# Kernel tuning notes

Measured on AMD Instinct MI355X. Metric: run time of the kernel, lower is better.

The kernel has to match this reference:

```python
import jax, jax.numpy as jnp
import numpy as np

B, N, DIM, VDIM, H, HD = 4, 1369, 1024, 1536, 16, 64
ROPE_HW, ROPE_DIM, THETA = 37, 32, 10000.0
LN_EPS = 1e-5


def _rope_tables():
    # VisionRotaryEmbeddingFast: freqs_for='lang', dim=32, pt_seq_len=ft_seq_len=37
    inv = 1.0 / THETA ** (jnp.arange(0, ROPE_DIM, 2, dtype=jnp.float32) / ROPE_DIM)  # [16]
    t = jnp.arange(ROPE_HW, dtype=jnp.float32) / ROPE_HW * ROPE_HW                    # [37]
    f = t[:, None] * inv[None, :]                                                     # [37,16]
    f = jnp.repeat(f, 2, axis=-1)                                                     # [37,32]
    # broadcat along last dim over the 2D grid -> [37,37,64]
    f2 = jnp.concatenate([jnp.broadcast_to(f[:, None, :], (ROPE_HW, ROPE_HW, ROPE_DIM)),
                          jnp.broadcast_to(f[None, :, :], (ROPE_HW, ROPE_HW, ROPE_DIM))], axis=-1)
    f2 = f2.reshape(-1, 2 * ROPE_DIM)                                                 # [1369,64]
    return jnp.cos(f2), jnp.sin(f2)


def _rotate_half(x):
    # pairs (x0,x1) -> (-x1,x0), interleaved
    xr = x.reshape(*x.shape[:-1], x.shape[-1] // 2, 2)
    x1, x2 = xr[..., 0], xr[..., 1]
    return jnp.stack((-x2, x1), axis=-1).reshape(x.shape)


def setup_inputs() -> dict:
    key = jax.random.key(0)
    ks = jax.random.split(key, 8)
    return {
        "x": jax.random.normal(ks[0], (B, N, DIM), jnp.float32),
        "value": jax.random.normal(ks[1], (B, N, VDIM), jnp.float32),
        "attn_mask": jax.random.randint(ks[2], (B, N), 0, 2).astype(bool),
        "wq": jax.random.normal(ks[3], (DIM, DIM), jnp.float32) * 0.02,
        "wk": jax.random.normal(ks[4], (DIM, VDIM), jnp.float32) * 0.02,
        "wv": jax.random.normal(ks[5], (DIM, VDIM), jnp.float32) * 0.02,
        "ln_g": jnp.ones((DIM,), jnp.float32),
        "ln_b": jnp.zeros((DIM,), jnp.float32),
        "wp": jax.random.normal(ks[6], (DIM, DIM), jnp.float32) * 0.02,
        "bp": jnp.zeros((DIM,), jnp.float32),
    }


def reference(x, value, attn_mask, wq, wk, wv, ln_g, ln_b, wp, bp):
    cos, sin = _rope_tables()  # [N, 64] each
    # projections (torch F.linear: y = x @ W.T)
    q = jnp.einsum('bni,oi->bno', x, wq).reshape(B, N, H, HD).transpose(0, 2, 1, 3)
    k = jnp.einsum('bni,oi->bno', value, wk).reshape(B, N, H, HD).transpose(0, 2, 1, 3)
    v = jnp.einsum('bni,oi->bno', value, wv).reshape(B, N, H, HD).transpose(0, 2, 1, 3)
    # inline RoPE on q and k
    q = q * cos + _rotate_half(q) * sin
    k = k * cos + _rotate_half(k) * sin
    q = q * (HD ** -0.5)
    attn = jnp.einsum('bhnd,bhmd->bhnm', q, k)
    neg_inf = jnp.finfo(attn.dtype).min
    attn = jnp.where(attn_mask[:, None, None, :], attn, neg_inf)
    attn = jax.nn.softmax(attn, axis=-1)
    out = jnp.einsum('bhnm,bhmd->bhnd', attn, v)
    out = out.transpose(0, 2, 1, 3).reshape(B, N, H * HD)
    # inner_attn_ln (LayerNorm, eps=1e-5)
    mu = jnp.mean(out, axis=-1, keepdims=True)
    var = jnp.var(out, axis=-1, keepdims=True)
    out = (out - mu) * jax.lax.rsqrt(var + LN_EPS) * ln_g + ln_b
    # output projection
    return jnp.einsum('bni,oi->bno', out, wp) + bp
```

## Files before the change

kernel.cpp:

```cpp
#include <hip/hip_runtime.h>
#include <hip/hip_bf16.h>

#define BB 4
#define NN 1369
#define DIMM 1024
#define VDIMM 1536
#define HH 16
#define MM (BB*NN)
#define MPAD 5504
#define NPAD 1408
#define KVB 64
#define NT (NPAD/KVB)

typedef __attribute__((ext_vector_type(4))) float f32x4;
typedef __attribute__((ext_vector_type(8))) __bf16 bf16x8;
typedef __attribute__((ext_vector_type(4))) __bf16 bf16x4;

#define GLOAD_LDS(gsrc, ldst) \
  __builtin_amdgcn_global_load_lds((const __attribute__((address_space(1))) unsigned int*)(gsrc), \
                                   (__attribute__((address_space(3))) unsigned int*)(ldst), 16, 0, 0)

__global__ __launch_bounds__(256) void cvt4(const float* __restrict__ src,
                                            __bf16* __restrict__ dst, int n4) {
  int i = blockIdx.x * blockDim.x + threadIdx.x;
  int st = gridDim.x * blockDim.x;
  for (; i < n4; i += st) {
    f32x4 v = ((const f32x4*)src)[i];
    bf16x4 o;
    o[0] = (__bf16)v[0]; o[1] = (__bf16)v[1];
    o[2] = (__bf16)v[2]; o[3] = (__bf16)v[3];
    ((bf16x4*)dst)[i] = o;
  }
}

__global__ __launch_bounds__(256) void rope_tables(float* __restrict__ cosT,
                                                   float* __restrict__ sinT) {
  int idx = blockIdx.x * blockDim.x + threadIdx.x;
  if (idx >= NN * 64) return;
  int n = idx >> 6, d = idx & 63;
  int r = n / 37, c = n % 37;
  int m = (d < 32) ? (d >> 1) : ((d - 32) >> 1);
  float p = (d < 32) ? (float)r : (float)c;
  float inv = powf(10000.f, -(float)m * (1.f / 16.f));
  float a = p * inv;
  cosT[idx] = cosf(a);
  sinT[idx] = sinf(a);
}

__global__ __launch_bounds__(256) void mask_prep(const void* __restrict__ mask,
                                                 float* __restrict__ maskA) {
  __shared__ int flags[2];
  int t = threadIdx.x;
  if (t < 2) flags[t] = 0;
  __syncthreads();
  const unsigned int* mw = (const unsigned int*)mask;
  for (int i = t; i < NN; i += blockDim.x) {
    unsigned int w = mw[i];
    if (w == 0x3F800000u) atomicOr(&flags[1], 1);
    else if (w > 1u) atomicOr(&flags[0], 1);
  }
  __syncthreads();
  int md = flags[1] ? 2 : (flags[0] ? 1 : 0);
  const unsigned char* mb = (const unsigned char*)mask;
  const float* mf = (const float*)mask;
  for (int i = t; i < BB * NPAD; i += blockDim.x) {
    int b = i / NPAD, key = i % NPAD;
    float v = -1e30f;
    if (key < NN) {
      int idx = b * NN + key;
      bool on = (md == 0) ? (mw[idx] != 0u) : (md == 1) ? (mb[idx] != 0) : (mf[idx] != 0.f);
      if (on) v = 0.f;
    }
    maskA[i] = v;
  }
}

template <int EPI>
__global__ __launch_bounds__(256) void gemm_bt(
    const __bf16* __restrict__ A, const __bf16* __restrict__ W, int K,
    __bf16* __restrict__ obf, float* __restrict__ of32,
    const float* __restrict__ cosT, const float* __restrict__ sinT,
    const float* __restrict__ bp) {
  __shared__ __bf16 As[128 * 32];
  __shared__ __bf16 Bs[128 * 32];
  const int tid = threadIdx.x;
  const int w = tid >> 6, l = tid & 63;
  const int tM = blockIdx.y, tN = blockIdx.x;
  const int wm = w >> 1, wn = w & 1;
  const int lo = l & 15, hi = l >> 4;

  f32x4 zero = {0.f, 0.f, 0.f, 0.f};
  f32x4 acc[4][4];
#pragma unroll
  for (int i = 0; i < 4; ++i)
#pragma unroll
    for (int j = 0; j < 4; ++j) acc[i][j] = zero;

  for (int k0 = 0; k0 < K; k0 += 32) {
    __syncthreads();
#pragma unroll
    for (int j = 0; j < 2; ++j) {
      int c = j * 4 + w;
      {
        const char* src = (const char*)A +
            ((size_t)(tM * 128 + c * 16 + (l >> 2)) * K + k0) * 2 + (l & 3) * 16;
        GLOAD_LDS(src, (char*)As + c * 1024);
      }
      {
        const char* src = (const char*)W +
            ((size_t)(tN * 128 + c * 16 + (l >> 2)) * K + k0) * 2 + (l & 3) * 16;
        GLOAD_LDS(src, (char*)Bs + c * 1024);
      }
    }
    __syncthreads();
    bf16x8 af[4], bfr[4];
#pragma unroll
    for (int mi = 0; mi < 4; ++mi)
      af[mi] = *(const bf16x8*)&As[(wm * 64 + mi * 16 + lo) * 32 + hi * 8];
#pragma unroll
    for (int ni = 0; ni < 4; ++ni)
      bfr[ni] = *(const bf16x8*)&Bs[(wn * 64 + ni * 16 + lo) * 32 + hi * 8];
#pragma unroll
    for (int mi = 0; mi < 4; ++mi)
#pragma unroll
      for (int ni = 0; ni < 4; ++ni)
        acc[mi][ni] = __builtin_amdgcn_mfma_f32_16x16x32_bf16(af[mi], bfr[ni], acc[mi][ni], 0, 0, 0);
  }

  const int m_base = tM * 128 + wm * 64;
  const int o_base = tN * 128 + wn * 64;
#pragma unroll
  for (int mi = 0; mi < 4; ++mi) {
#pragma unroll
    for (int r = 0; r < 4; ++r) {
      const int mrow = m_base + mi * 16 + hi * 4 + r;
#pragma unroll
      for (int ni = 0; ni < 4; ++ni) {
        const int col = o_base + ni * 16 + lo;
        float v = acc[mi][ni][r];
        if (EPI == 0 || EPI == 1) {
          float pprt = __shfl_xor(v, 1);
          if (mrow < MM) {
            int b = mrow / NN, n = mrow % NN;
            int h = col >> 6, d = col & 63;
            float cs = cosT[n * 64 + d], sn = sinT[n * 64 + d];
            float out = v * cs + (((d & 1) == 0) ? -pprt : pprt) * sn;
            if (EPI == 0) out *= 0.125f;
            obf[((size_t)(b * HH + h) * NPAD + n) * 64 + d] = (__bf16)out;
          }
        } else if (EPI == 2) {
          if (mrow < MM) {
            int b = mrow / NN, n = mrow % NN;
            int h = col >> 6, d = col & 63;
            obf[((size_t)(b * HH + h) * 64 + d) * NPAD + n] = (__bf16)v;
          }
        } else {
          if (mrow < MM) of32[(size_t)mrow * DIMM + col] = v + bp[col];
        }
      }
    }
  }
}

__device__ inline unsigned int pk2(float a, float b) {
  unsigned int ua = (unsigned int)__builtin_bit_cast(unsigned short, (__bf16)a);
  unsigned int ub = (unsigned int)__builtin_bit_cast(unsigned short, (__bf16)b);
  return ua | (ub << 16);
}

__global__ __launch_bounds__(256) void attn_kernel(
    const __bf16* __restrict__ Qb, const __bf16* __restrict__ Kb,
    const __bf16* __restrict__ Vtb, const float* __restrict__ maskA,
    float* __restrict__ AO) {
  __shared__ __bf16 Ks[2][64 * 64];
  __shared__ __bf16 Vs[2][64 * 64];
  __shared__ unsigned int Plds[4][16 * 32];
  const int tid = threadIdx.x;
  const int w = tid >> 6, l = tid & 63;
  const int lo = l & 15, hi = l >> 4;

  const int i = blockIdx.x;
  const int orig = (i & 7) * 176 + (i >> 3);
  const int bh = orig / NT;
  const int qt = orig % NT;
  const int b = bh >> 4;
  const int q0 = qt * 64 + w * 16;

  const __bf16* Qp = Qb + ((size_t)bh * NPAD + q0) * 64;
  bf16x8 qf0 = *(const bf16x8*)&Qp[lo * 64 + hi * 8];
  bf16x8 qf1 = *(const bf16x8*)&Qp[lo * 64 + 32 + hi * 8];

  const int row8 = l >> 3;
  const int swz16 = ((l & 7) ^ row8) << 4;
  const int lo7 = lo & 7;
  const int swzW = (lo & 7) << 2;

  f32x4 zero = {0.f, 0.f, 0.f, 0.f};
  f32x4 O[4];
#pragma unroll
  for (int n = 0; n < 4; ++n) O[n] = zero;
  float lr = 0.f;
  const float* mk = maskA + b * NPAD;

#define STAGE(buf, k0)                                                                   \
  {                                                                                      \
    _Pragma("unroll") for (int j = 0; j < 2; ++j) {                                      \
      const int rbase = (j * 4 + w) * 8;                                                 \
      const char* ksrc = (const char*)Kb +                                               \
          ((size_t)bh * NPAD + (k0) + rbase + row8) * 128 + swz16;                       \
      GLOAD_LDS(ksrc, (char*)&Ks[buf][0] + rbase * 128);                                 \
      const char* vsrc = (const char*)Vtb +                                              \
          ((size_t)(bh * 64 + rbase + row8) * NPAD + (k0)) * 2 + swz16;                  \
      GLOAD_LDS(vsrc, (char*)&Vs[buf][0] + rbase * 128);                                 \
    }                                                                                    \
  }

  STAGE(0, 0);
  __syncthreads();
  int cur = 0;

  for (int t = 0; t < NT; ++t) {
    if (t + 1 < NT) STAGE(cur ^ 1, (t + 1) * KVB);

    const __bf16* KB = &Ks[cur][0];
    const __bf16* VB = &Vs[cur][0];

    f32x4 mv[4];
#pragma unroll
    for (int c = 0; c < 4; ++c) mv[c] = *(const f32x4*)&mk[t * KVB + c * 16 + hi * 4];

    f32x4 S[4];
    __builtin_amdgcn_s_setprio(1);
#pragma unroll
    for (int c = 0; c < 4; ++c) {
      const int kr = c * 16 + lo;
      bf16x8 kfa = *(const bf16x8*)&KB[kr * 64 + ((hi ^ lo7) * 8)];
      bf16x8 kfb = *(const bf16x8*)&KB[kr * 64 + (((hi + 4) ^ lo7) * 8)];
      f32x4 s = __builtin_amdgcn_mfma_f32_16x16x32_bf16(kfa, qf0, zero, 0, 0, 0);
      S[c]     = __builtin_amdgcn_mfma_f32_16x16x32_bf16(kfb, qf1, s, 0, 0, 0);
    }
    __builtin_amdgcn_s_setprio(0);

    float rs = 0.f;
#pragma unroll
    for (int c = 0; c < 4; ++c) {
      float p0 = __expf(S[c][0] + mv[c][0]);
      float p1 = __expf(S[c][1] + mv[c][1]);
      float p2 = __expf(S[c][2] + mv[c][2]);
      float p3 = __expf(S[c][3] + mv[c][3]);
      rs += (p0 + p1) + (p2 + p3);
      uint2 pw = {pk2(p0, p1), pk2(p2, p3)};
      *(uint2*)&Plds[w][lo * 32 + ((8 * c + 2 * hi) ^ swzW)] = pw;
    }
    lr += rs;

    bf16x8 pf0 = *(const bf16x8*)&Plds[w][lo * 32 + ((4 * hi) ^ swzW)];
    bf16x8 pf1 = *(const bf16x8*)&Plds[w][lo * 32 + ((16 + 4 * hi) ^ swzW)];

    __builtin_amdgcn_s_setprio(1);
#pragma unroll
    for (int n = 0; n < 4; ++n) {
      const int vr = n * 16 + lo;
      bf16x8 vfa = *(const bf16x8*)&VB[vr * 64 + ((hi ^ lo7) * 8)];
      bf16x8 vfb = *(const bf16x8*)&VB[vr * 64 + (((hi + 4) ^ lo7) * 8)];
      O[n] = __builtin_amdgcn_mfma_f32_16x16x32_bf16(vfa, pf0, O[n], 0, 0, 0);
      O[n] = __builtin_amdgcn_mfma_f32_16x16x32_bf16(vfb, pf1, O[n], 0, 0, 0);
    }
    __builtin_amdgcn_s_setprio(0);

    __syncthreads();
    cur ^= 1;
  }
#undef STAGE

  lr += __shfl_xor(lr, 16);
  lr += __shfl_xor(lr, 32);
  const float inv = 1.f / lr;

  const int h = bh & 15;
  const int token = q0 + lo;
  if (token < NN) {
    float* dst = AO + (size_t)(b * NN + token) * DIMM + h * 64 + hi * 4;
#pragma unroll
    for (int n = 0; n < 4; ++n) {
      f32x4 o = O[n];
      o[0] *= inv; o[1] *= inv; o[2] *= inv; o[3] *= inv;
      *(f32x4*)(dst + n * 16) = o;
    }
  }
}

__global__ __launch_bounds__(256) void ln_kernel(
    const float* __restrict__ AO, const float* __restrict__ g,
    const float* __restrict__ be, __bf16* __restrict__ outb) {
  const int row = blockIdx.x;
  const int t = threadIdx.x;
  const float* x = AO + (size_t)row * DIMM;
  f32x4 v = ((const f32x4*)x)[t];
  float s = v[0] + v[1] + v[2] + v[3];
  float sq = v[0] * v[0] + v[1] * v[1] + v[2] * v[2] + v[3] * v[3];
#pragma unroll
  for (int m = 1; m < 64; m <<= 1) { s += __shfl_xor(s, m); sq += __shfl_xor(sq, m); }
  __shared__ float ss[4], ssq[4];
  int w = t >> 6, l = t & 63;
  if (l == 0) { ss[w] = s; ssq[w] = sq; }
  __syncthreads();
  s = ss[0] + ss[1] + ss[2] + ss[3];
  sq = ssq[0] + ssq[1] + ssq[2] + ssq[3];
  float mean = s * (1.f / 1024.f);
  float var = sq * (1.f / 1024.f) - mean * mean;
  float rstd = rsqrtf(var + 1e-5f);
  __bf16* o = outb + (size_t)row * DIMM + t * 4;
  const float* gp = g + t * 4;
  const float* bp2 = be + t * 4;
#pragma unroll
  for (int j = 0; j < 4; ++j) o[j] = (__bf16)((v[j] - mean) * rstd * gp[j] + bp2[j]);
}

extern "C" void kernel_launch(void* const* d_in, const int* in_sizes, int n_in,
                              void* d_out, int out_size, void* d_ws, size_t ws_size,
                              hipStream_t stream) {
  const float* x   = (const float*)d_in[0];
  const float* val = (const float*)d_in[1];
  const void*  msk = d_in[2];
  const float* wq  = (const float*)d_in[3];
  const float* wk  = (const float*)d_in[4];
  const float* wv  = (const float*)d_in[5];
  const float* lng = (const float*)d_in[6];
  const float* lnb = (const float*)d_in[7];
  const float* wp  = (const float*)d_in[8];
  const float* bpv = (const float*)d_in[9];
  float* out = (float*)d_out;

  char* ws = (char*)d_ws;
  size_t off = 0;
  auto alloc = [&](size_t bytes) -> char* {
    char* p = ws + off;
    off += (bytes + 255) & ~(size_t)255;
    return p;
  };
  __bf16* xb  = (__bf16*)alloc((size_t)MPAD * 1024 * 2);
  __bf16* vb  = (__bf16*)alloc((size_t)MPAD * 1536 * 2);
  __bf16* wqb = (__bf16*)alloc((size_t)1024 * 1024 * 2);
  __bf16* wkb = (__bf16*)alloc((size_t)1024 * 1536 * 2);
  __bf16* wvb = (__bf16*)alloc((size_t)1024 * 1536 * 2);
  __bf16* wpb = (__bf16*)alloc((size_t)1024 * 1024 * 2);
  __bf16* Qb  = (__bf16*)alloc((size_t)64 * NPAD * 64 * 2);
  __bf16* Kb  = (__bf16*)alloc((size_t)64 * NPAD * 64 * 2);
  __bf16* Vtb = (__bf16*)alloc((size_t)64 * 64 * NPAD * 2);
  float* AO   = (float*)alloc((size_t)MM * 1024 * 4);
  float* cosT = (float*)alloc((size_t)NN * 64 * 4);
  float* sinT = (float*)alloc((size_t)NN * 64 * 4);
  float* maskA = (float*)alloc((size_t)BB * NPAD * 4);

  hipMemsetAsync(xb + (size_t)MM * 1024, 0, (size_t)(MPAD - MM) * 1024 * 2, stream);
  hipMemsetAsync(vb + (size_t)MM * 1536, 0, (size_t)(MPAD - MM) * 1536 * 2, stream);
  hipMemsetAsync(Qb, 0, (size_t)64 * NPAD * 64 * 2, stream);
  hipMemsetAsync(Kb, 0, (size_t)64 * NPAD * 64 * 2, stream);
  hipMemsetAsync(Vtb, 0, (size_t)64 * 64 * NPAD * 2, stream);

  cvt4<<<1024, 256, 0, stream>>>(x, xb, MM * 1024 / 4);
  cvt4<<<1024, 256, 0, stream>>>(val, vb, MM * 1536 / 4);
  cvt4<<<512, 256, 0, stream>>>(wq, wqb, 1024 * 1024 / 4);
  cvt4<<<512, 256, 0, stream>>>(wk, wkb, 1024 * 1536 / 4);
  cvt4<<<512, 256, 0, stream>>>(wv, wvb, 1024 * 1536 / 4);
  cvt4<<<512, 256, 0, stream>>>(wp, wpb, 1024 * 1024 / 4);
  rope_tables<<<(NN * 64 + 255) / 256, 256, 0, stream>>>(cosT, sinT);
  mask_prep<<<1, 256, 0, stream>>>(msk, maskA);

  dim3 gg(8, 43);
  gemm_bt<0><<<gg, 256, 0, stream>>>(xb, wqb, 1024, Qb, nullptr, cosT, sinT, nullptr);
  gemm_bt<1><<<gg, 256, 0, stream>>>(vb, wkb, 1536, Kb, nullptr, cosT, sinT, nullptr);
  gemm_bt<2><<<gg, 256, 0, stream>>>(vb, wvb, 1536, Vtb, nullptr, nullptr, nullptr, nullptr);

  attn_kernel<<<dim3(64 * NT), 256, 0, stream>>>(Qb, Kb, Vtb, maskA, AO);

  ln_kernel<<<MM, 256, 0, stream>>>(AO, lng, lnb, xb);

  gemm_bt<3><<<gg, 256, 0, stream>>>(xb, wpb, 1024, nullptr, out, nullptr, nullptr, bpv);
}
```

Baseline: 314.1 us.

## Fuse K and V projections into one GEMM, use 64-wide tiles, exp2 softmax

The separate K and V projection GEMMs become one GEMM over a concatenated [2048,1536] weight. Its epilogue sends columns below 1024 to the RoPE'd K output and the rest to the transposed V output. The Q and output-projection GEMMs switch to 128x64 tiles, giving a 16x43 grid that fills more CUs. The Q scale now folds in log2(e), so the attention softmax can use exp2f instead of __expf. Smaller tiles mean each block reuses less data per load.

```diff
diff --git a/kernel.cpp b/kernel.cpp
--- a/kernel.cpp
+++ b/kernel.cpp
@@ -11,6 +11,7 @@
 #define NPAD 1408
 #define KVB 64
 #define NT (NPAD/KVB)
+#define QSCALE 0.18028334f
 
 typedef __attribute__((ext_vector_type(4))) float f32x4;
 typedef __attribute__((ext_vector_type(8))) __bf16 bf16x8;
@@ -75,24 +76,28 @@
   }
 }
 
-template <int EPI>
+template <int TN, int EPI>
 __global__ __launch_bounds__(256) void gemm_bt(
     const __bf16* __restrict__ A, const __bf16* __restrict__ W, int K,
-    __bf16* __restrict__ obf, float* __restrict__ of32,
+    __bf16* __restrict__ obf, __bf16* __restrict__ obf2, float* __restrict__ of32,
     const float* __restrict__ cosT, const float* __restrict__ sinT,
     const float* __restrict__ bp) {
+  constexpr int MI = (TN == 128) ? 4 : 2;
   __shared__ __bf16 As[128 * 32];
-  __shared__ __bf16 Bs[128 * 32];
+  __shared__ __bf16 Bs[TN * 32];
   const int tid = threadIdx.x;
   const int w = tid >> 6, l = tid & 63;
   const int tM = blockIdx.y, tN = blockIdx.x;
-  const int wm = w >> 1, wn = w & 1;
+  const int wm = (TN == 128) ? (w >> 1) : w;
+  const int wn = (TN == 128) ? (w & 1) : 0;
+  const int wmo = wm * ((TN == 128) ? 64 : 32);
+  const int wno = wn * 64;
   const int lo = l & 15, hi = l >> 4;
 
   f32x4 zero = {0.f, 0.f, 0.f, 0.f};
-  f32x4 acc[4][4];
-#pragma unroll
-  for (int i = 0; i < 4; ++i)
+  f32x4 acc[MI][4];
+#pragma unroll
+  for (int i = 0; i < MI; ++i)
 #pragma unroll
     for (int j = 0; j < 4; ++j) acc[i][j] = zero;
 
@@ -101,36 +106,43 @@
 #pragma unroll
     for (int j = 0; j < 2; ++j) {
       int c = j * 4 + w;
-      {
-        const char* src = (const char*)A +
-            ((size_t)(tM * 128 + c * 16 + (l >> 2)) * K + k0) * 2 + (l & 3) * 16;
-        GLOAD_LDS(src, (char*)As + c * 1024);
-      }
-      {
+      const char* src = (const char*)A +
+          ((size_t)(tM * 128 + c * 16 + (l >> 2)) * K + k0) * 2 + (l & 3) * 16;
+      GLOAD_LDS(src, (char*)As + c * 1024);
+    }
+    if (TN == 128) {
+#pragma unroll
+      for (int j = 0; j < 2; ++j) {
+        int c = j * 4 + w;
         const char* src = (const char*)W +
             ((size_t)(tN * 128 + c * 16 + (l >> 2)) * K + k0) * 2 + (l & 3) * 16;
         GLOAD_LDS(src, (char*)Bs + c * 1024);
       }
+    } else {
+      const char* src = (const char*)W +
+          ((size_t)(tN * 64 + w * 16 + (l >> 2)) * K + k0) * 2 + (l & 3) * 16;
+      GLOAD_LDS(src, (char*)Bs + w * 1024);
     }
     __syncthreads();
-    bf16x8 af[4], bfr[4];
-#pragma unroll
-    for (int mi = 0; mi < 4; ++mi)
-      af[mi] = *(const bf16x8*)&As[(wm * 64 + mi * 16 + lo) * 32 + hi * 8];
+    bf16x8 af[MI], bfr[4];
+#pragma unroll
+    for (int mi = 0; mi < MI; ++mi)
+      af[mi] = *(const bf16x8*)&As[(wmo + mi * 16 + lo) * 32 + hi * 8];
 #pragma unroll
     for (int ni = 0; ni < 4; ++ni)
-      bfr[ni] = *(const bf16x8*)&Bs[(wn * 64 + ni * 16 + lo) * 32 + hi * 8];
-#pragma unroll
-    for (int mi = 0; mi < 4; ++mi)
+      bfr[ni] = *(const bf16x8*)&Bs[(wno + ni * 16 + lo) * 32 + hi * 8];
+#pragma unroll
+    for (int mi = 0; mi < MI; ++mi)
 #pragma unroll
       for (int ni = 0; ni < 4; ++ni)
         acc[mi][ni] = __builtin_amdgcn_mfma_f32_16x16x32_bf16(af[mi], bfr[ni], acc[mi][ni], 0, 0, 0);
   }
 
-  const int m_base = tM * 128 + wm * 64;
-  const int o_base = tN * 128 + wn * 64;
-#pragma unroll
-  for (int mi = 0; mi < 4; ++mi) {
+  const int m_base = tM * 128 + wmo;
+  const int o_base = tN * TN + wno;
+  const bool isK = (EPI == 1) && (tN * TN < 1024);
+#pragma unroll
+  for (int mi = 0; mi < MI; ++mi) {
 #pragma unroll
     for (int r = 0; r < 4; ++r) {
       const int mrow = m_base + mi * 16 + hi * 4 + r;
@@ -138,21 +150,32 @@
       for (int ni = 0; ni < 4; ++ni) {
         const int col = o_base + ni * 16 + lo;
         float v = acc[mi][ni][r];
-        if (EPI == 0 || EPI == 1) {
+        if (EPI == 0) {
           float pprt = __shfl_xor(v, 1);
           if (mrow < MM) {
             int b = mrow / NN, n = mrow % NN;
             int h = col >> 6, d = col & 63;
             float cs = cosT[n * 64 + d], sn = sinT[n * 64 + d];
-            float out = v * cs + (((d & 1) == 0) ? -pprt : pprt) * sn;
-            if (EPI == 0) out *= 0.125f;
+            float out = (v * cs + (((d & 1) == 0) ? -pprt : pprt) * sn) * QSCALE;
             obf[((size_t)(b * HH + h) * NPAD + n) * 64 + d] = (__bf16)out;
           }
-        } else if (EPI == 2) {
-          if (mrow < MM) {
-            int b = mrow / NN, n = mrow % NN;
-            int h = col >> 6, d = col & 63;
-            obf[((size_t)(b * HH + h) * 64 + d) * NPAD + n] = (__bf16)v;
+        } else if (EPI == 1) {
+          if (isK) {
+            float pprt = __shfl_xor(v, 1);
+            if (mrow < MM) {
+              int b = mrow / NN, n = mrow % NN;
+              int h = col >> 6, d = col & 63;
+              float cs = cosT[n * 64 + d], sn = sinT[n * 64 + d];
+              float out = v * cs + (((d & 1) == 0) ? -pprt : pprt) * sn;
+              obf[((size_t)(b * HH + h) * NPAD + n) * 64 + d] = (__bf16)out;
+            }
+          } else {
+            if (mrow < MM) {
+              int b = mrow / NN, n = mrow % NN;
+              int o2 = col - 1024;
+              int h = o2 >> 6, d = o2 & 63;
+              obf2[((size_t)(b * HH + h) * 64 + d) * NPAD + n] = (__bf16)v;
+            }
           }
         } else {
           if (mrow < MM) of32[(size_t)mrow * DIMM + col] = v + bp[col];
@@ -244,10 +267,10 @@
     float rs = 0.f;
 #pragma unroll
     for (int c = 0; c < 4; ++c) {
-      float p0 = __expf(S[c][0] + mv[c][0]);
-      float p1 = __expf(S[c][1] + mv[c][1]);
-      float p2 = __expf(S[c][2] + mv[c][2]);
-      float p3 = __expf(S[c][3] + mv[c][3]);
+      float p0 = exp2f(S[c][0] + mv[c][0]);
+      float p1 = exp2f(S[c][1] + mv[c][1]);
+      float p2 = exp2f(S[c][2] + mv[c][2]);
+      float p3 = exp2f(S[c][3] + mv[c][3]);
       rs += (p0 + p1) + (p2 + p3);
       uint2 pw = {pk2(p0, p1), pk2(p2, p3)};
       *(uint2*)&Plds[w][lo * 32 + ((8 * c + 2 * hi) ^ swzW)] = pw;
@@ -339,18 +362,17 @@
     off += (bytes + 255) & ~(size_t)255;
     return p;
   };
-  __bf16* xb  = (__bf16*)alloc((size_t)MPAD * 1024 * 2);
-  __bf16* vb  = (__bf16*)alloc((size_t)MPAD * 1536 * 2);
-  __bf16* wqb = (__bf16*)alloc((size_t)1024 * 1024 * 2);
-  __bf16* wkb = (__bf16*)alloc((size_t)1024 * 1536 * 2);
-  __bf16* wvb = (__bf16*)alloc((size_t)1024 * 1536 * 2);
-  __bf16* wpb = (__bf16*)alloc((size_t)1024 * 1024 * 2);
-  __bf16* Qb  = (__bf16*)alloc((size_t)64 * NPAD * 64 * 2);
-  __bf16* Kb  = (__bf16*)alloc((size_t)64 * NPAD * 64 * 2);
-  __bf16* Vtb = (__bf16*)alloc((size_t)64 * 64 * NPAD * 2);
-  float* AO   = (float*)alloc((size_t)MM * 1024 * 4);
-  float* cosT = (float*)alloc((size_t)NN * 64 * 4);
-  float* sinT = (float*)alloc((size_t)NN * 64 * 4);
+  __bf16* xb   = (__bf16*)alloc((size_t)MPAD * 1024 * 2);
+  __bf16* vb   = (__bf16*)alloc((size_t)MPAD * 1536 * 2);
+  __bf16* wqb  = (__bf16*)alloc((size_t)1024 * 1024 * 2);
+  __bf16* wkvb = (__bf16*)alloc((size_t)2048 * 1536 * 2);
+  __bf16* wpb  = (__bf16*)alloc((size_t)1024 * 1024 * 2);
+  __bf16* Qb   = (__bf16*)alloc((size_t)64 * NPAD * 64 * 2);
+  __bf16* Kb   = (__bf16*)alloc((size_t)64 * NPAD * 64 * 2);
+  __bf16* Vtb  = (__bf16*)alloc((size_t)64 * 64 * NPAD * 2);
+  float* AO    = (float*)alloc((size_t)MM * 1024 * 4);
+  float* cosT  = (float*)alloc((size_t)NN * 64 * 4);
+  float* sinT  = (float*)alloc((size_t)NN * 64 * 4);
   float* maskA = (float*)alloc((size_t)BB * NPAD * 4);
 
   hipMemsetAsync(xb + (size_t)MM * 1024, 0, (size_t)(MPAD - MM) * 1024 * 2, stream);
@@ -362,20 +384,18 @@
   cvt4<<<1024, 256, 0, stream>>>(x, xb, MM * 1024 / 4);
   cvt4<<<1024, 256, 0, stream>>>(val, vb, MM * 1536 / 4);
   cvt4<<<512, 256, 0, stream>>>(wq, wqb, 1024 * 1024 / 4);
-  cvt4<<<512, 256, 0, stream>>>(wk, wkb, 1024 * 1536 / 4);
-  cvt4<<<512, 256, 0, stream>>>(wv, wvb, 1024 * 1536 / 4);
+  cvt4<<<512, 256, 0, stream>>>(wk, wkvb, 1024 * 1536 / 4);
+  cvt4<<<512, 256, 0, stream>>>(wv, wkvb + (size_t)1024 * 1536, 1024 * 1536 / 4);
   cvt4<<<512, 256, 0, stream>>>(wp, wpb, 1024 * 1024 / 4);
   rope_tables<<<(NN * 64 + 255) / 256, 256, 0, stream>>>(cosT, sinT);
   mask_prep<<<1, 256, 0, stream>>>(msk, maskA);
 
-  dim3 gg(8, 43);
-  gemm_bt<0><<<gg, 256, 0, stream>>>(xb, wqb, 1024, Qb, nullptr, cosT, sinT, nullptr);
-  gemm_bt<1><<<gg, 256, 0, stream>>>(vb, wkb, 1536, Kb, nullptr, cosT, sinT, nullptr);
-  gemm_bt<2><<<gg, 256, 0, stream>>>(vb, wvb, 1536, Vtb, nullptr, nullptr, nullptr, nullptr);
+  gemm_bt<64, 0><<<dim3(16, 43), 256, 0, stream>>>(xb, wqb, 1024, Qb, nullptr, nullptr, cosT, sinT, nullptr);
+  gemm_bt<128, 1><<<dim3(16, 43), 256, 0, stream>>>(vb, wkvb, 1536, Kb, Vtb, nullptr, cosT, sinT, nullptr);
 
   attn_kernel<<<dim3(64 * NT), 256, 0, stream>>>(Qb, Kb, Vtb, maskA, AO);
 
   ln_kernel<<<MM, 256, 0, stream>>>(AO, lng, lnb, xb);
 
-  gemm_bt<3><<<gg, 256, 0, stream>>>(xb, wpb, 1024, nullptr, out, nullptr, nullptr, bpv);
-}
+  gemm_bt<64, 3><<<dim3(16, 43), 256, 0, stream>>>(xb, wpb, 1024, nullptr, nullptr, out, nullptr, nullptr, bpv);
+}
```

New measurement: 303.0 us. 3.6% less time.
